# Performance work log

Measured on AMD Instinct MI355X. Metric: run time of the kernel, lower is better.

Reference implementation:

```python
import jax, jax.numpy as jnp
import numpy as np

S, TM1, B, V, E, H = 96, 96, 8, 32000, 256, 512
PAD = 0
NEG = -1e30


def setup_inputs() -> dict:
    key = jax.random.key(0)
    ks = jax.random.split(key, 10)
    n = lambda k, shape, s=0.05: (jax.random.normal(k, shape, jnp.float32) * s)
    return {
        "src": jax.random.randint(ks[0], (S, B), 0, V, jnp.int32),
        "tgt": jax.random.randint(ks[1], (TM1 + 1, B), 0, V, jnp.int32),
        "emb": n(ks[2], (V, E)),
        "W_ih": n(ks[3], (4 * H, E)),
        "W_hh": n(ks[4], (4 * H, H)),
        "b_ih": jnp.zeros((4 * H,), jnp.float32),
        "b_hh": jnp.zeros((4 * H,), jnp.float32),
        "W_att": n(ks[5], (H, H)),
        "sent": n(ks[6], (H,)),
        "W_read": n(ks[7], (V, H)),
    }


def _lstm_cell(x, h, c, W_ih, W_hh, b_ih, b_hh):
    g = x @ W_ih.T + b_ih + h @ W_hh.T + b_hh
    i, f, gg, o = jnp.split(g, 4, axis=-1)
    c = jax.nn.sigmoid(f) * c + jax.nn.sigmoid(i) * jnp.tanh(gg)
    h = jax.nn.sigmoid(o) * jnp.tanh(c)
    return h, c


def _forward(src, tgt, emb, W_ih, W_hh, b_ih, b_hh, W_att, sent, W_read):
    # padding_idx behavior: pad row of embedding is zero (and gets no grad)
    emb_eff = emb * (jnp.arange(V) != PAD).astype(emb.dtype)[:, None]
    xs = jnp.concatenate([emb_eff[src], emb_eff[tgt[:-1]]], axis=0)  # [S+TM1,B,E]

    def step(carry, x):
        h, c = carry
        h, c = _lstm_cell(x, h, c, W_ih, W_hh, b_ih, b_hh)
        return (h, c), h

    init = (jnp.zeros((B, H), xs.dtype), jnp.zeros((B, H), xs.dtype))
    _, H_all = jax.lax.scan(step, init, xs)  # [S+TM1,B,H]

    H_dec = H_all[S:]                              # [TM1,B,H]
    Q = jnp.tanh(H_dec @ W_att.T)                  # [TM1,B,H]
    Z = jnp.einsum("tbh,jbh->tjb", Q, H_all)      # [TM1,S+TM1,B]
    zs = jnp.einsum("tbh,h->tb", Q, sent)         # sentinel logit
    logits = jnp.concatenate([Z, zs[:, None, :]], axis=1)  # [TM1,S+TM1+1,B]

    j = jnp.arange(S + TM1 + 1)
    t = jnp.arange(TM1)
    valid = (j[None, :] < S + t[:, None] + 1) | (j[None, :] == S + TM1)
    logits = jnp.where(valid[:, :, None], logits, NEG)
    a = jax.nn.softmax(logits, axis=1)
    a_src, a_tgt, a_sent = a[:, :S], a[:, S:S + TM1], a[:, -1]

    # pointer distributions via scatter-add (avoids dense one-hot [S,B,V])
    b_idx = jnp.arange(B)[None, None, :]
    t_idx = jnp.arange(TM1)[:, None, None]
    p_ptr = jnp.zeros((TM1, B, V), a.dtype)
    p_ptr = p_ptr.at[t_idx, b_idx, src[None, :, :]].add(a_src)
    p_ptr = p_ptr.at[t_idx, b_idx, tgt[:-1][None, :, :]].add(a_tgt)

    p_vocab = jax.nn.softmax(H_dec @ W_read.T, axis=-1)  # [TM1,B,V]
    p = p_ptr + p_vocab * a_sent[:, :, None]
    ptr_scores = p_ptr + a_sent[:, :, None]

    mask = (tgt != PAD).astype(p.dtype)  # [TM1+1,B]
    gold = jnp.take_along_axis(jnp.log(p), tgt[1:][:, :, None], axis=2)[..., 0] * mask[1:]
    gold_ptr = jnp.take_along_axis(jnp.log(ptr_scores), tgt[1:][:, :, None], axis=2)[..., 0] * mask[1:]
    return gold.sum(0), gold_ptr.sum(0)  # ([B], [B])


def reference(src, tgt, emb, W_ih, W_hh, b_ih, b_hh, W_att, sent, W_read):
    return _forward(src, tgt, emb, W_ih, W_hh, b_ih, b_hh, W_att, sent, W_read)
```

## Files before the change

kernel.cpp:

```cpp
#include <hip/hip_runtime.h>
#include <math.h>

#define SS   96
#define TM   96
#define BB   8
#define VV   32000
#define EE   256
#define HH   512
#define NTOK (SS + TM)
#define G4   (4 * HH)
#define NEGF (-1e30f)
#define LBLK 16

typedef __attribute__((ext_vector_type(8))) short short8;
typedef __attribute__((ext_vector_type(4))) float f32x4;
typedef __attribute__((ext_vector_type(4))) unsigned uint32x4;
typedef unsigned long long u64;

#define XIH_OFF   ((size_t)0)
#define XIH_SZ    ((size_t)NTOK * BB * G4)
#define HALL_OFF  (XIH_OFF + XIH_SZ)
#define HALL_SZ   ((size_t)NTOK * BB * HH)
#define Q_OFF     (HALL_OFF + HALL_SZ)
#define Q_SZ      ((size_t)TM * BB * HH)
#define PPTR_OFF  (Q_OFF + Q_SZ)
#define ASENT_OFF (PPTR_OFF + (size_t)(TM * BB))
#define SSUM_OFF  (ASENT_OFF + (size_t)(TM * BB))
#define LSTAR_OFF (SSUM_OFF + (size_t)(TM * BB))
#define FLAG_OFF  (LSTAR_OFF + (size_t)(TM * BB))
#define HBF_OFF   (FLAG_OFF + (size_t)1024)
#define HBF_SZF   ((size_t)2 * BB * HH / 2)
#define WHHBF_OFF (HBF_OFF + HBF_SZF)
#define WHHBF_SZF ((size_t)G4 * HH / 2)
#define ABF_OFF   (WHHBF_OFF + WHHBF_SZF)
#define ABF_SZF   ((size_t)(TM * BB) * HH / 2)
#define WBF_OFF   (ABF_OFF + ABF_SZF)
#define WBF_SZF   ((size_t)VV * HH / 2)
#define NEED_F    (WBF_OFF + WBF_SZF)

__device__ __forceinline__ float sigf(float x) { return 1.f / (1.f + __expf(-x)); }

__device__ __forceinline__ unsigned short f2bf(float x) {
    unsigned bits = __float_as_uint(x);
    bits += 0x7FFFu + ((bits >> 16) & 1u);
    return (unsigned short)(bits >> 16);
}

__global__ void __launch_bounds__(256) k_xih(const int* __restrict__ src,
                                             const int* __restrict__ tgt,
                                             const float* __restrict__ emb,
                                             const float* __restrict__ Wih,
                                             const float* __restrict__ bih,
                                             const float* __restrict__ bhh,
                                             float* __restrict__ xih) {
    __shared__ float xs[16][EE];
    const int tok0 = blockIdx.x * 16;
    const int row0 = blockIdx.y * 256;
    const int tid  = threadIdx.x;

    for (int e = tid; e < 16 * EE; e += 256) {
        int tk = e >> 8, k = e & 255;
        int tau = tok0 + tk;
        int idx = (tau < SS * BB) ? src[tau] : tgt[tau - SS * BB];
        xs[tk][k] = (idx == 0) ? 0.f : emb[(size_t)idx * EE + k];
    }
    __syncthreads();

    const int row = row0 + tid;
    const float bias = bih[row] + bhh[row];
    float acc[16];
#pragma unroll
    for (int r = 0; r < 16; ++r) acc[r] = bias;

    const float4* w4 = (const float4*)(Wih + (size_t)row * EE);
    for (int k4 = 0; k4 < EE / 4; ++k4) {
        float4 w = w4[k4];
#pragma unroll
        for (int r = 0; r < 16; ++r) {
            float4 x = *((const float4*)&xs[r][k4 * 4]);
            acc[r] += w.x * x.x + w.y * x.y + w.z * x.z + w.w * x.w;
        }
    }
#pragma unroll
    for (int r = 0; r < 16; ++r)
        xih[(size_t)(tok0 + r) * G4 + row] = acc[r];
}

__global__ void __launch_bounds__(256) k_cvt2(const float* __restrict__ src,
                                              unsigned short* __restrict__ dst,
                                              long n) {
    size_t base = ((size_t)blockIdx.x * 256 + threadIdx.x) * 8;
    if ((long)base >= n) return;
    float4 f0 = *(const float4*)(src + base);
    float4 f1 = *(const float4*)(src + base + 4);
    uint4 o;
    o.x = (unsigned)f2bf(f0.x) | ((unsigned)f2bf(f0.y) << 16);
    o.y = (unsigned)f2bf(f0.z) | ((unsigned)f2bf(f0.w) << 16);
    o.z = (unsigned)f2bf(f1.x) | ((unsigned)f2bf(f1.y) << 16);
    o.w = (unsigned)f2bf(f1.z) | ((unsigned)f2bf(f1.w) << 16);
    *(uint4*)(dst + base) = o;
}

__global__ void __launch_bounds__(256, 1) k_lstm(const float* __restrict__ xih,
                                                 const unsigned short* __restrict__ whhbf,
                                                 float* __restrict__ hall,
                                                 unsigned short* __restrict__ hbf,
                                                 unsigned short* __restrict__ abf,
                                                 unsigned* __restrict__ flags) {
    extern __shared__ short lA[];
    const int tid = threadIdx.x;
    const int wv  = tid >> 6;
    const int l   = tid & 63;
    const int b16 = l & 15;
    const int kg  = l >> 4;
    const int bb  = b16 & 7;
    const int bx  = blockIdx.x;
    const int I0  = bx * 32 + wv * 8;

    const int j = b16;
    const unsigned short* a0p = whhbf + ((size_t)((j >> 3) * HH + I0 + (j & 7))) * HH + kg * 8;
    const unsigned short* a1p = whhbf + ((size_t)((2 + (j >> 3)) * HH + I0 + (j & 7))) * HH + kg * 8;
    short* lA0 = lA + (((size_t)wv * 2 + 0) * 16 * 64 + l) * 8;
    short* lA1 = lA + (((size_t)wv * 2 + 1) * 16 * 64 + l) * 8;
#pragma unroll
    for (int ks = 0; ks < 16; ++ks) {
        *(short8*)(lA0 + ks * 512) = *(const short8*)(a0p + ks * 32);
        *(short8*)(lA1 + ks * 512) = *(const short8*)(a1p + ks * 32);
    }
    __syncthreads();

    const int xgate0 = (kg >> 1);
    const int xgate1 = 2 + (kg >> 1);
    const int xi     = I0 + (kg & 1) * 4;

    float c0[4] = {0.f, 0.f, 0.f, 0.f};
    union fragu { uint32x4 u4; short8 s; };

    for (int t = 0; t < NTOK; ++t) {
        const float* xb = xih + ((size_t)t * BB + bb) * G4;
        float4 x0 = *(const float4*)(xb + xgate0 * HH + xi);
        float4 x1 = *(const float4*)(xb + xgate1 * HH + xi);

        fragu Bf[16];
        if (t > 0) {
            if (l < 16) {
                while (__hip_atomic_load(&flags[(size_t)l * 16], __ATOMIC_RELAXED,
                                         __HIP_MEMORY_SCOPE_AGENT) < (unsigned)t) {}
            }
            const unsigned short* hsrc =
                hbf + ((t - 1) & 1) * (BB * HH) + (size_t)bb * HH + kg * 8;
#pragma unroll
            for (int ks = 0; ks < 16; ++ks)
                asm volatile("global_load_dwordx4 %0, %1, off sc0 sc1"
                             : "=v"(Bf[ks].u4) : "v"(hsrc + ks * 32) : "memory");
            asm volatile("s_waitcnt vmcnt(0)" ::: "memory");
            __builtin_amdgcn_sched_barrier(0);
        }

        f32x4 acc0 = {x0.x, x0.y, x0.z, x0.w};
        f32x4 acc1 = {x1.x, x1.y, x1.z, x1.w};
        if (t > 0) {
#pragma unroll
            for (int ks = 0; ks < 16; ++ks) {
                short8 a0 = *(const short8*)(lA0 + ks * 512);
                short8 a1 = *(const short8*)(lA1 + ks * 512);
                acc0 = __builtin_amdgcn_mfma_f32_16x16x32_bf16(a0, Bf[ks].s, acc0, 0, 0, 0);
                acc1 = __builtin_amdgcn_mfma_f32_16x16x32_bf16(a1, Bf[ks].s, acc1, 0, 0, 0);
            }
        }

        float hreg[4];
#pragma unroll
        for (int r = 0; r < 4; ++r) {
            float gf = __shfl_down(acc0[r], 32, 64);
            float go = __shfl_down(acc1[r], 32, 64);
            float is = sigf(acc0[r]);
            float fs = sigf(gf);
            float gv = tanhf(acc1[r]);
            float os = sigf(go);
            c0[r] = fs * c0[r] + is * gv;
            hreg[r] = os * tanhf(c0[r]);
        }

        if (l < 32 && b16 < BB) {
            const int ib = I0 + kg * 4;
            *(float4*)(hall + ((size_t)t * BB + b16) * HH + ib) =
                make_float4(hreg[0], hreg[1], hreg[2], hreg[3]);
            u64 pk = (u64)f2bf(hreg[0]) | ((u64)f2bf(hreg[1]) << 16) |
                     ((u64)f2bf(hreg[2]) << 32) | ((u64)f2bf(hreg[3]) << 48);
            if (t >= SS)
                *(u64*)(abf + ((size_t)(t - SS) * BB + b16) * HH + ib) = pk;
            if (t < NTOK - 1) {
                unsigned short* hdst = hbf + (t & 1) * (BB * HH) + (size_t)b16 * HH + ib;
                asm volatile("global_store_dwordx2 %0, %1, off sc0 sc1"
                             :: "v"(hdst), "v"(pk) : "memory");
            }
        }

        if (t < NTOK - 1) {
            asm volatile("s_waitcnt vmcnt(0)" ::: "memory");
            __syncthreads();
            if (tid == 0)
                __hip_atomic_store(&flags[(size_t)bx * 16], (unsigned)(t + 1),
                                   __ATOMIC_RELAXED, __HIP_MEMORY_SCOPE_AGENT);
        }
    }
}

__global__ void __launch_bounds__(256) k_q(const float* __restrict__ hall,
                                           const float* __restrict__ Watt,
                                           float* __restrict__ q) {
    __shared__ float hb[8 * 516];
    const int t = blockIdx.x, tid = threadIdx.x;
    const float* hdec = hall + (size_t)(SS + t) * (BB * HH);
    for (int e = tid; e < BB * HH; e += 256)
        hb[(e >> 9) * 516 + (e & 511)] = hdec[e];
    __syncthreads();

    for (int oi = tid; oi < BB * HH; oi += 256) {
        int b = oi & 7, ii = oi >> 3;
        const float4* w4 = (const float4*)(Watt + (size_t)ii * HH);
        const float4* h4 = (const float4*)(hb + b * 516);
        float acc = 0.f;
        for (int k4 = 0; k4 < HH / 4; ++k4) {
            float4 w = w4[k4], h = h4[k4];
            acc += w.x * h.x + w.y * h.y + w.z * h.z + w.w * h.w;
        }
        q[(size_t)(t * BB + b) * HH + ii] = tanhf(acc);
    }
}

__global__ void __launch_bounds__(256) k_att(const float* __restrict__ hall,
                                             const float* __restrict__ q,
                                             const float* __restrict__ sent,
                                             const int* __restrict__ src,
                                             const int* __restrict__ tgt,
                                             float* __restrict__ pptr,
                                             float* __restrict__ asent) {
    __shared__ float qs[HH];
    __shared__ float av[256];
    __shared__ float red[256];
    const int t = blockIdx.x, b = blockIdx.y, tid = threadIdx.x;

    for (int e = tid; e < HH; e += 256) qs[e] = q[(size_t)(t * BB + b) * HH + e];
    __syncthreads();

    const int j = tid;
    float acc = NEGF;
    if (j < SS + TM + 1) {
        bool valid = (j < SS + t + 1) || (j == SS + TM);
        if (valid) {
            const float* vptr = (j < SS + TM) ? (hall + (size_t)(j * BB + b) * HH) : sent;
            const float4* v4 = (const float4*)vptr;
            const float4* q4 = (const float4*)qs;
            float a = 0.f;
            for (int k4 = 0; k4 < HH / 4; ++k4) {
                float4 v = v4[k4], qq = q4[k4];
                a += v.x * qq.x + v.y * qq.y + v.z * qq.z + v.w * qq.w;
            }
            acc = a;
        }
    }
    red[tid] = acc;
    __syncthreads();
    for (int s2 = 128; s2 > 0; s2 >>= 1) {
        if (tid < s2) red[tid] = fmaxf(red[tid], red[tid + s2]);
        __syncthreads();
    }
    float m = red[0];
    __syncthreads();
    float e = __expf(acc - m);
    red[tid] = e;
    __syncthreads();
    for (int s2 = 128; s2 > 0; s2 >>= 1) {
        if (tid < s2) red[tid] += red[tid + s2];
        __syncthreads();
    }
    float denom = red[0];
    __syncthreads();
    float a = e / denom;
    av[tid] = a;
    __syncthreads();

    const int vs = tgt[(t + 1) * BB + b];
    float contrib = 0.f;
    if (j < SS) {
        if (src[j * BB + b] == vs) contrib += av[j];
        if (tgt[j * BB + b] == vs) contrib += av[SS + j];
    }
    red[tid] = contrib;
    __syncthreads();
    for (int s2 = 128; s2 > 0; s2 >>= 1) {
        if (tid < s2) red[tid] += red[tid + s2];
        __syncthreads();
    }
    if (tid == 0) {
        pptr[t * BB + b]  = red[0];
        asent[t * BB + b] = av[SS + TM];
    }
}

__global__ void __launch_bounds__(256) k_vocab_mfma(const unsigned short* __restrict__ Abf,
                                                    const unsigned short* __restrict__ Wbf,
                                                    const int* __restrict__ tgt,
                                                    float* __restrict__ ssum,
                                                    float* __restrict__ lstar) {
    const int tid  = threadIdx.x;
    const int wave = tid >> 6;
    const int lane = tid & 63;
    const int r16  = lane & 15;
    const int kg   = lane >> 4;
    const int n0   = blockIdx.x * 64;

    const unsigned short* b0 = Wbf + (size_t)(n0 +  0 + r16) * HH + kg * 8;
    const unsigned short* b1 = Wbf + (size_t)(n0 + 16 + r16) * HH + kg * 8;
    const unsigned short* b2 = Wbf + (size_t)(n0 + 32 + r16) * HH + kg * 8;
    const unsigned short* b3 = Wbf + (size_t)(n0 + 48 + r16) * HH + kg * 8;

    for (int pass = 0; pass < 12; ++pass) {
        const int row0 = pass * 64 + wave * 16;
        const unsigned short* arow = Abf + (size_t)(row0 + r16) * HH + kg * 8;

        f32x4 acc0 = {0.f,0.f,0.f,0.f}, acc1 = acc0, acc2 = acc0, acc3 = acc0;
#pragma unroll
        for (int ks = 0; ks < 16; ++ks) {
            short8 a = *(const short8*)(arow + ks * 32);
            acc0 = __builtin_amdgcn_mfma_f32_16x16x32_bf16(a, *(const short8*)(b0 + ks * 32), acc0, 0, 0, 0);
            acc1 = __builtin_amdgcn_mfma_f32_16x16x32_bf16(a, *(const short8*)(b1 + ks * 32), acc1, 0, 0, 0);
            acc2 = __builtin_amdgcn_mfma_f32_16x16x32_bf16(a, *(const short8*)(b2 + ks * 32), acc2, 0, 0, 0);
            acc3 = __builtin_amdgcn_mfma_f32_16x16x32_bf16(a, *(const short8*)(b3 + ks * 32), acc3, 0, 0, 0);
        }

#pragma unroll
        for (int reg = 0; reg < 4; ++reg) {
            const int rowg = row0 + 4 * kg + reg;
            const int vs = tgt[BB + rowg];
            int cg;
            cg = n0 +  0 + r16; if (cg == vs) lstar[rowg] = acc0[reg];
            cg = n0 + 16 + r16; if (cg == vs) lstar[rowg] = acc1[reg];
            cg = n0 + 32 + r16; if (cg == vs) lstar[rowg] = acc2[reg];
            cg = n0 + 48 + r16; if (cg == vs) lstar[rowg] = acc3[reg];

            float v = __expf(acc0[reg]) + __expf(acc1[reg]) +
                      __expf(acc2[reg]) + __expf(acc3[reg]);
            v += __shfl_xor(v, 1, 64);
            v += __shfl_xor(v, 2, 64);
            v += __shfl_xor(v, 4, 64);
            v += __shfl_xor(v, 8, 64);
            if (r16 == 0) atomicAdd(&ssum[rowg], v);
        }
    }
}

__global__ void __launch_bounds__(256) k_vocab_f32(const float* __restrict__ hall,
                                                   const float* __restrict__ Wread,
                                                   const int* __restrict__ tgt,
                                                   float* __restrict__ ssum,
                                                   float* __restrict__ lstar) {
    __shared__ float hs[32 * HH];
    const int tid = threadIdx.x;
    const int v0 = blockIdx.x * 512 + tid * 2;
    const int v1 = v0 + 1;
    const bool g0 = v0 < VV, g1 = v1 < VV;
    const float4* w40 = (const float4*)(Wread + (size_t)(g0 ? v0 : 0) * HH);
    const float4* w41 = (const float4*)(Wread + (size_t)(g1 ? v1 : 0) * HH);
    const int rbase0 = blockIdx.y * 128;

    for (int ch = 0; ch < 4; ++ch) {
        const int rbase = rbase0 + ch * 32;
        const float4* sp4 = (const float4*)(hall + ((size_t)SS * BB + rbase) * HH);
        float4* hs4 = (float4*)hs;
        for (int e = tid; e < 32 * HH / 4; e += 256) hs4[e] = sp4[e];
        __syncthreads();

        float acc0[32], acc1[32];
#pragma unroll
        for (int r = 0; r < 32; ++r) { acc0[r] = 0.f; acc1[r] = 0.f; }

        for (int k4 = 0; k4 < HH / 4; ++k4) {
            float4 w0 = w40[k4];
            float4 w1 = w41[k4];
#pragma unroll
            for (int r = 0; r < 32; ++r) {
                float4 h = *((const float4*)(hs + r * HH + k4 * 4));
                acc0[r] += w0.x * h.x + w0.y * h.y + w0.z * h.z + w0.w * h.w;
                acc1[r] += w1.x * h.x + w1.y * h.y + w1.z * h.z + w1.w * h.w;
            }
        }

#pragma unroll
        for (int r = 0; r < 32; ++r) {
            const int row = rbase + r;
            float val = 0.f;
            if (g0) val += __expf(acc0[r]);
            if (g1) val += __expf(acc1[r]);
#pragma unroll
            for (int d = 32; d > 0; d >>= 1) val += __shfl_xor(val, d, 64);
            if ((tid & 63) == 0) atomicAdd(&ssum[row], val);
            const int vs = tgt[row + BB];
            if (g0 && v0 == vs) lstar[row] = acc0[r];
            else if (g1 && v1 == vs) lstar[row] = acc1[r];
        }
        __syncthreads();
    }
}

__global__ void __launch_bounds__(768) k_final(const float* __restrict__ pptr,
                                               const float* __restrict__ asent,
                                               const float* __restrict__ ssum,
                                               const float* __restrict__ lstar,
                                               const int* __restrict__ tgt,
                                               float* __restrict__ out) {
    __shared__ float g[TM * BB], gp[TM * BB];
    const int tid = threadIdx.x;
    const int vs = tgt[tid + BB];
    const float pv = __expf(lstar[tid]) / ssum[tid];
    const float ps = pptr[tid];
    const float as = asent[tid];
    if (vs != 0) {
        g[tid]  = logf(ps + pv * as);
        gp[tid] = logf(ps + as);
    } else {
        g[tid] = 0.f; gp[tid] = 0.f;
    }
    __syncthreads();
    if (tid < BB) {
        float s1 = 0.f, s2 = 0.f;
        for (int t = 0; t < TM; ++t) { s1 += g[t * BB + tid]; s2 += gp[t * BB + tid]; }
        out[tid] = s1;
        out[BB + tid] = s2;
    }
}

extern "C" void kernel_launch(void* const* d_in, const int* in_sizes, int n_in,
                              void* d_out, int out_size, void* d_ws, size_t ws_size,
                              hipStream_t stream) {
    (void)in_sizes; (void)n_in; (void)out_size;
    const int*   src   = (const int*)d_in[0];
    const int*   tgt   = (const int*)d_in[1];
    const float* emb   = (const float*)d_in[2];
    const float* Wih   = (const float*)d_in[3];
    const float* Whh   = (const float*)d_in[4];
    const float* bih   = (const float*)d_in[5];
    const float* bhh   = (const float*)d_in[6];
    const float* Watt  = (const float*)d_in[7];
    const float* sent  = (const float*)d_in[8];
    const float* Wread = (const float*)d_in[9];
    float* ws  = (float*)d_ws;
    float* out = (float*)d_out;

    const bool use_mfma_vocab = ws_size >= NEED_F * sizeof(float);

    (void)hipMemsetAsync((void*)(ws + SSUM_OFF), 0, (size_t)2560 * sizeof(float), stream);

    k_xih<<<dim3(NTOK * BB / 16, G4 / 256), 256, 0, stream>>>(
        src, tgt, emb, Wih, bih, bhh, ws + XIH_OFF);

    k_cvt2<<<dim3((unsigned)((size_t)G4 * HH / 8 / 256)), 256, 0, stream>>>(
        Whh, (unsigned short*)(ws + WHHBF_OFF), (long)G4 * HH);

    {
        const float* xih = ws + XIH_OFF;
        const unsigned short* whhbf = (const unsigned short*)(ws + WHHBF_OFF);
        float* hall = ws + HALL_OFF;
        unsigned short* hbf = (unsigned short*)(ws + HBF_OFF);
        unsigned short* abf = (unsigned short*)(ws + ABF_OFF);
        unsigned* flags = (unsigned*)(ws + FLAG_OFF);
        void* args[] = { (void*)&xih, (void*)&whhbf, (void*)&hall,
                         (void*)&hbf, (void*)&abf, (void*)&flags };
        (void)hipLaunchCooperativeKernel((void*)k_lstm, dim3(LBLK), dim3(256), args,
                                         131072, stream);
    }

    k_q<<<dim3(TM), 256, 0, stream>>>(ws + HALL_OFF, Watt, ws + Q_OFF);

    k_att<<<dim3(TM, BB), 256, 0, stream>>>(ws + HALL_OFF, ws + Q_OFF, sent,
                                            src, tgt, ws + PPTR_OFF, ws + ASENT_OFF);

    if (use_mfma_vocab) {
        k_cvt2<<<dim3((unsigned)((size_t)VV * HH / 8 / 256)), 256, 0, stream>>>(
            Wread, (unsigned short*)(ws + WBF_OFF), (long)VV * HH);
        k_vocab_mfma<<<dim3(VV / 64), 256, 0, stream>>>(
            (const unsigned short*)(ws + ABF_OFF),
            (const unsigned short*)(ws + WBF_OFF),
            tgt, ws + SSUM_OFF, ws + LSTAR_OFF);
    } else {
        k_vocab_f32<<<dim3(63, 6), 256, 0, stream>>>(ws + HALL_OFF, Wread, tgt,
                                                     ws + SSUM_OFF, ws + LSTAR_OFF);
    }

    k_final<<<dim3(1), dim3(TM * BB), 0, stream>>>(ws + PPTR_OFF, ws + ASENT_OFF,
                                                   ws + SSUM_OFF, ws + LSTAR_OFF,
                                                   tgt, out);
}
```

Before: 1.339 ms.

## Merge prep kernels into one launch and use per-wave LSTM step flags

```diff
diff --git a/kernel.cpp b/kernel.cpp
--- a/kernel.cpp
+++ b/kernel.cpp
@@ -11,6 +11,11 @@
 #define G4   (4 * HH)
 #define NEGF (-1e30f)
 #define LBLK 16
+
+#define NXIH  768
+#define NCVTW 512
+#define NCVTR 8000
+#define NPREP (NXIH + NCVTW + NCVTR)
 
 typedef __attribute__((ext_vector_type(8))) short short8;
 typedef __attribute__((ext_vector_type(4))) float f32x4;
@@ -46,59 +51,66 @@
     return (unsigned short)(bits >> 16);
 }
 
-__global__ void __launch_bounds__(256) k_xih(const int* __restrict__ src,
-                                             const int* __restrict__ tgt,
-                                             const float* __restrict__ emb,
-                                             const float* __restrict__ Wih,
-                                             const float* __restrict__ bih,
-                                             const float* __restrict__ bhh,
-                                             float* __restrict__ xih) {
-    __shared__ float xs[16][EE];
-    const int tok0 = blockIdx.x * 16;
-    const int row0 = blockIdx.y * 256;
-    const int tid  = threadIdx.x;
-
-    for (int e = tid; e < 16 * EE; e += 256) {
-        int tk = e >> 8, k = e & 255;
-        int tau = tok0 + tk;
-        int idx = (tau < SS * BB) ? src[tau] : tgt[tau - SS * BB];
-        xs[tk][k] = (idx == 0) ? 0.f : emb[(size_t)idx * EE + k];
-    }
-    __syncthreads();
-
-    const int row = row0 + tid;
-    const float bias = bih[row] + bhh[row];
-    float acc[16];
-#pragma unroll
-    for (int r = 0; r < 16; ++r) acc[r] = bias;
-
-    const float4* w4 = (const float4*)(Wih + (size_t)row * EE);
-    for (int k4 = 0; k4 < EE / 4; ++k4) {
-        float4 w = w4[k4];
-#pragma unroll
-        for (int r = 0; r < 16; ++r) {
-            float4 x = *((const float4*)&xs[r][k4 * 4]);
-            acc[r] += w.x * x.x + w.y * x.y + w.z * x.z + w.w * x.w;
-        }
-    }
-#pragma unroll
-    for (int r = 0; r < 16; ++r)
-        xih[(size_t)(tok0 + r) * G4 + row] = acc[r];
-}
-
-__global__ void __launch_bounds__(256) k_cvt2(const float* __restrict__ src,
-                                              unsigned short* __restrict__ dst,
-                                              long n) {
-    size_t base = ((size_t)blockIdx.x * 256 + threadIdx.x) * 8;
-    if ((long)base >= n) return;
-    float4 f0 = *(const float4*)(src + base);
-    float4 f1 = *(const float4*)(src + base + 4);
+__global__ void __launch_bounds__(256) k_prep(const int* __restrict__ src,
+                                              const int* __restrict__ tgt,
+                                              const float* __restrict__ emb,
+                                              const float* __restrict__ Wih,
+                                              const float* __restrict__ bih,
+                                              const float* __restrict__ bhh,
+                                              const float* __restrict__ Whh,
+                                              const float* __restrict__ Wread,
+                                              float* __restrict__ xih,
+                                              unsigned short* __restrict__ whhbf,
+                                              unsigned short* __restrict__ wbf) {
+    __shared__ float xs[16 * EE];
+    const int bid = blockIdx.x;
+    const int tid = threadIdx.x;
+
+    if (bid < NXIH) {
+        const int tok0 = (bid >> 3) * 16;
+        const int row0 = (bid & 7) * 256;
+        for (int e = tid; e < 16 * EE; e += 256) {
+            int tk = e >> 8, k = e & 255;
+            int tau = tok0 + tk;
+            int idx = (tau < SS * BB) ? src[tau] : tgt[tau - SS * BB];
+            xs[tk * EE + k] = (idx == 0) ? 0.f : emb[(size_t)idx * EE + k];
+        }
+        __syncthreads();
+
+        const int row = row0 + tid;
+        const float bias = bih[row] + bhh[row];
+        float acc[16];
+#pragma unroll
+        for (int r = 0; r < 16; ++r) acc[r] = bias;
+        const float4* w4 = (const float4*)(Wih + (size_t)row * EE);
+        for (int k4 = 0; k4 < EE / 4; ++k4) {
+            float4 w = w4[k4];
+#pragma unroll
+            for (int r = 0; r < 16; ++r) {
+                float4 x = *((const float4*)&xs[r * EE + k4 * 4]);
+                acc[r] += w.x * x.x + w.y * x.y + w.z * x.z + w.w * x.w;
+            }
+        }
+#pragma unroll
+        for (int r = 0; r < 16; ++r)
+            xih[(size_t)(tok0 + r) * G4 + row] = acc[r];
+        return;
+    }
+
+    const float* srcp;
+    unsigned short* dstp;
+    size_t base;
+    if (bid < NXIH + NCVTW) { srcp = Whh;   dstp = whhbf; base = (size_t)(bid - NXIH) * 2048; }
+    else                    { srcp = Wread; dstp = wbf;   base = (size_t)(bid - NXIH - NCVTW) * 2048; }
+    base += (size_t)tid * 8;
+    float4 f0 = *(const float4*)(srcp + base);
+    float4 f1 = *(const float4*)(srcp + base + 4);
     uint4 o;
     o.x = (unsigned)f2bf(f0.x) | ((unsigned)f2bf(f0.y) << 16);
     o.y = (unsigned)f2bf(f0.z) | ((unsigned)f2bf(f0.w) << 16);
     o.z = (unsigned)f2bf(f1.x) | ((unsigned)f2bf(f1.y) << 16);
     o.w = (unsigned)f2bf(f1.z) | ((unsigned)f2bf(f1.w) << 16);
-    *(uint4*)(dst + base) = o;
+    *(uint4*)(dstp + base) = o;
 }
 
 __global__ void __launch_bounds__(256, 1) k_lstm(const float* __restrict__ xih,
@@ -116,6 +128,7 @@
     const int bb  = b16 & 7;
     const int bx  = blockIdx.x;
     const int I0  = bx * 32 + wv * 8;
+    unsigned* myflag = flags + (size_t)(bx * 4 + wv) * 16;
 
     const int j = b16;
     const unsigned short* a0p = whhbf + ((size_t)((j >> 3) * HH + I0 + (j & 7))) * HH + kg * 8;
@@ -143,10 +156,9 @@
 
         fragu Bf[16];
         if (t > 0) {
-            if (l < 16) {
-                while (__hip_atomic_load(&flags[(size_t)l * 16], __ATOMIC_RELAXED,
-                                         __HIP_MEMORY_SCOPE_AGENT) < (unsigned)t) {}
-            }
+            while (__hip_atomic_load(&flags[(size_t)l * 16], __ATOMIC_RELAXED,
+                                     __HIP_MEMORY_SCOPE_AGENT) < (unsigned)t) {}
+
             const unsigned short* hsrc =
                 hbf + ((t - 1) & 1) * (BB * HH) + (size_t)bb * HH + kg * 8;
 #pragma unroll
@@ -199,9 +211,8 @@
 
         if (t < NTOK - 1) {
             asm volatile("s_waitcnt vmcnt(0)" ::: "memory");
-            __syncthreads();
-            if (tid == 0)
-                __hip_atomic_store(&flags[(size_t)bx * 16], (unsigned)(t + 1),
+            if (l == 0)
+                __hip_atomic_store(myflag, (unsigned)(t + 1),
                                    __ATOMIC_RELAXED, __HIP_MEMORY_SCOPE_AGENT);
         }
     }
@@ -453,11 +464,9 @@
 
     (void)hipMemsetAsync((void*)(ws + SSUM_OFF), 0, (size_t)2560 * sizeof(float), stream);
 
-    k_xih<<<dim3(NTOK * BB / 16, G4 / 256), 256, 0, stream>>>(
-        src, tgt, emb, Wih, bih, bhh, ws + XIH_OFF);
-
-    k_cvt2<<<dim3((unsigned)((size_t)G4 * HH / 8 / 256)), 256, 0, stream>>>(
-        Whh, (unsigned short*)(ws + WHHBF_OFF), (long)G4 * HH);
+    k_prep<<<dim3(NPREP), 256, 0, stream>>>(
+        src, tgt, emb, Wih, bih, bhh, Whh, Wread,
+        ws + XIH_OFF, (unsigned short*)(ws + WHHBF_OFF), (unsigned short*)(ws + WBF_OFF));
 
     {
         const float* xih = ws + XIH_OFF;
@@ -478,8 +487,6 @@
                                             src, tgt, ws + PPTR_OFF, ws + ASENT_OFF);
 
     if (use_mfma_vocab) {
-        k_cvt2<<<dim3((unsigned)((size_t)VV * HH / 8 / 256)), 256, 0, stream>>>(
-            Wread, (unsigned short*)(ws + WBF_OFF), (long)VV * HH);
         k_vocab_mfma<<<dim3(VV / 64), 256, 0, stream>>>(
             (const unsigned short*)(ws + ABF_OFF),
             (const unsigned short*)(ws + WBF_OFF),
```

Result: slower. 1.420 ms (+6.0%).
